# Optimization experiments

Measured on AMD Instinct MI355X. Metric: run time of the kernel, lower is better.

The kernel has to match this reference:

```python
import jax, jax.numpy as jnp
import numpy as np

D_MODEL, D_K, D_V = 1024, 128, 128


def setup_inputs() -> dict:
    key = jax.random.key(0)
    kx, kq, kk, kv = jax.random.split(key, 4)
    B, T = 8, 2048
    x = jax.random.normal(kx, (B, T, D_MODEL), dtype=jnp.float32)
    # nn.Linear(d_model, d_out, bias=False): weight [d_out, d_model], y = x @ W.T
    s = 1.0 / np.sqrt(D_MODEL)
    Wq = jax.random.uniform(kq, (D_K, D_MODEL), jnp.float32, -s, s)
    Wk = jax.random.uniform(kk, (D_K, D_MODEL), jnp.float32, -s, s)
    Wv = jax.random.uniform(kv, (D_V, D_MODEL), jnp.float32, -s, s)
    return {"x": x, "Wq": Wq, "Wk": Wk, "Wv": Wv}


def reference(x, Wq, Wk, Wv):
    B, T, C = x.shape
    Q = jnp.einsum('btc,kc->btk', x, Wq)  # [B,T,d_k]
    K = jnp.einsum('btc,kc->btk', x, Wk)  # [B,T,d_k]
    V = jnp.einsum('btc,vc->btv', x, Wv)  # [B,T,d_v]
    scores = jnp.einsum('bqk,btk->bqt', Q, K) / jnp.sqrt(jnp.float32(D_K))  # [B,T,T]
    causal = jnp.tril(jnp.ones((T, T), dtype=bool))
    scores = jnp.where(causal, scores, -jnp.inf)
    probs = jax.nn.softmax(scores, axis=2)
    return jnp.einsum('bqt,btv->bqv', probs, V)
```

## Files before the change

### kernel.cpp

```cpp
#include <hip/hip_runtime.h>
#include <hip/hip_bf16.h>

#define BATCH 8
#define TDIM  2048
#define CDIM  1024
#define DDIM  128

typedef float  f32x4  __attribute__((ext_vector_type(4)));
typedef __bf16 bf16x8 __attribute__((ext_vector_type(8)));
typedef unsigned short u16;
typedef unsigned int   u32;
typedef u16 u16x4 __attribute__((ext_vector_type(4)));
typedef u16 u16x8 __attribute__((ext_vector_type(8)));
typedef u32 u32x4 __attribute__((ext_vector_type(4)));

static __device__ __forceinline__ u16 f2bf(float f) {
    union { float f; unsigned int u; } cv;
    cv.f = f;
    unsigned int lsb = (cv.u >> 16) & 1u;
    cv.u += 0x7fffu + lsb;
    return (u16)(cv.u >> 16);
}

static __device__ __forceinline__ float bf2f(u16 v) {
    union { u32 u; float f; } cv;
    cv.u = (u32)v << 16;
    return cv.f;
}

static __device__ __forceinline__ u32 packbf(float a, float b) {
    return (u32)f2bf(a) | ((u32)f2bf(b) << 16);
}

static __device__ __forceinline__ void gload16(const u16* g, u16* l) {
    __builtin_amdgcn_global_load_lds(
        (const __attribute__((address_space(1))) void*)g,
        (__attribute__((address_space(3))) void*)l, 16, 0, 0);
}

__global__ __launch_bounds__(256) void convert_w(
    const float* __restrict__ Wq, const float* __restrict__ Wk,
    const float* __restrict__ Wv, u16* __restrict__ wb)
{
    const int which = blockIdx.x >> 4;
    const int kb    = blockIdx.x & 15;
    const float* W = (which == 0) ? Wq : (which == 1) ? Wk : Wv;
    u16* dst = wb + ((size_t)(which * 16 + kb)) * 8192;
    const int t = threadIdx.x;
    for (int i = 0; i < 4; ++i) {
        int j   = i * 256 + t;
        int row = j & 127;
        int cb  = (j >> 7) & 3;
        int kk2 = j >> 9;
        const float* s = &W[(size_t)row * CDIM + kb * 64 + kk2 * 32 + cb * 8];
        f32x4 a = *reinterpret_cast<const f32x4*>(s);
        f32x4 b = *reinterpret_cast<const f32x4*>(s + 4);
        u16x8 o;
        o[0] = f2bf(a[0]); o[1] = f2bf(a[1]); o[2] = f2bf(a[2]); o[3] = f2bf(a[3]);
        o[4] = f2bf(b[0]); o[5] = f2bf(b[1]); o[6] = f2bf(b[2]); o[7] = f2bf(b[3]);
        *reinterpret_cast<u16x8*>(dst + (size_t)j * 8) = o;
    }
}

__global__ __launch_bounds__(256) void qkv_gemm(
    const float* __restrict__ x, const u16* __restrict__ wb,
    u16* __restrict__ Qw, u16* __restrict__ Ktl, u16* __restrict__ Vtl)
{
    __shared__ alignas(16) u16 As[4096];
    __shared__ alignas(16) u16 Bs[8192];

    const int bid   = blockIdx.x;
    const int which = bid >> 8;
    const int mt    = bid & 255;
    const int rbase = mt * 64;
    const u16* Bb = wb + (size_t)which * 131072;

    const int tid  = threadIdx.x;
    const int wid  = tid >> 6;
    const int lane = tid & 63;
    const int g    = lane >> 4;
    const int lr   = lane & 15;
    const int wc   = wid * 32;

    const int arow = tid >> 2;
    const int aseg = tid & 3;
    const int abase = (aseg >> 1) * 2048 + (aseg & 1) * 1024 + arow * 8;

    f32x4 acc[4][2] = {};

    for (int kb = 0; kb < 16; ++kb) {
        const float* ax = &x[(size_t)(rbase + arow) * CDIM + kb * 64 + aseg * 16];
        f32x4 v0 = *reinterpret_cast<const f32x4*>(ax);
        f32x4 v1 = *reinterpret_cast<const f32x4*>(ax + 4);
        f32x4 v2 = *reinterpret_cast<const f32x4*>(ax + 8);
        f32x4 v3 = *reinterpret_cast<const f32x4*>(ax + 12);
        u16x8 p0, p1;
        p0[0]=f2bf(v0[0]); p0[1]=f2bf(v0[1]); p0[2]=f2bf(v0[2]); p0[3]=f2bf(v0[3]);
        p0[4]=f2bf(v1[0]); p0[5]=f2bf(v1[1]); p0[6]=f2bf(v1[2]); p0[7]=f2bf(v1[3]);
        p1[0]=f2bf(v2[0]); p1[1]=f2bf(v2[1]); p1[2]=f2bf(v2[2]); p1[3]=f2bf(v2[3]);
        p1[4]=f2bf(v3[0]); p1[5]=f2bf(v3[1]); p1[6]=f2bf(v3[2]); p1[7]=f2bf(v3[3]);
        *reinterpret_cast<u16x8*>(&As[abase])       = p0;
        *reinterpret_cast<u16x8*>(&As[abase + 512]) = p1;
        const u16* Bt = Bb + (size_t)kb * 8192;
        for (int i = 0; i < 4; ++i)
            gload16(Bt + (size_t)(i * 256 + tid) * 8, &Bs[(i * 256 + wid * 64) * 8]);
        __syncthreads();

        bf16x8 af[2][4], bf[2][2];
        for (int kk2 = 0; kk2 < 2; ++kk2) {
            for (int mi = 0; mi < 4; ++mi)
                af[kk2][mi] = __builtin_bit_cast(bf16x8, *reinterpret_cast<const u16x8*>(
                    &As[kk2 * 2048 + g * 512 + (mi * 16 + lr) * 8]));
            for (int ni = 0; ni < 2; ++ni)
                bf[kk2][ni] = __builtin_bit_cast(bf16x8, *reinterpret_cast<const u16x8*>(
                    &Bs[kk2 * 4096 + g * 1024 + (wc + ni * 16 + lr) * 8]));
        }
        for (int kk2 = 0; kk2 < 2; ++kk2)
            for (int mi = 0; mi < 4; ++mi)
                for (int ni = 0; ni < 2; ++ni)
                    acc[mi][ni] = __builtin_amdgcn_mfma_f32_16x16x32_bf16(
                        af[kk2][mi], bf[kk2][ni], acc[mi][ni], 0, 0, 0);
        __syncthreads();
    }

    const int b  = mt >> 5;
    const int kt = mt & 31;
    if (which == 0) {
        const float sc = 0.08838834764831845f;
        for (int mi = 0; mi < 4; ++mi)
            for (int ni = 0; ni < 2; ++ni) {
                int row = mi * 16 + g * 4;
                int col = wc + ni * 16 + lr;
                for (int r = 0; r < 4; ++r)
                    Bs[(row + r) * 128 + col] = f2bf(acc[mi][ni][r] * sc);
            }
        __syncthreads();
        u16* dst = Qw + (size_t)rbase * DDIM;
        for (int i = 0; i < 4; ++i)
            *reinterpret_cast<u16x8*>(&dst[(size_t)(i * 256 + tid) * 8]) =
                *reinterpret_cast<const u16x8*>(&Bs[(i * 256 + tid) * 8]);
    } else if (which == 1) {
        for (int mi = 0; mi < 4; ++mi)
            for (int ni = 0; ni < 2; ++ni) {
                int row = mi * 16 + g * 4;
                int col = wc + ni * 16 + lr;
                int ebase = (col >> 5) * 2048 + ((col >> 3) & 3) * 512 + (col & 7);
                for (int r = 0; r < 4; ++r)
                    Bs[ebase + (row + r) * 8] = f2bf(acc[mi][ni][r]);
            }
        __syncthreads();
        u16* dst = Ktl + ((size_t)(b * 32 + kt)) * 8192;
        for (int i = 0; i < 4; ++i)
            *reinterpret_cast<u16x8*>(&dst[(size_t)(i * 256 + tid) * 8]) =
                *reinterpret_cast<const u16x8*>(&Bs[(i * 256 + tid) * 8]);
    } else {
        for (int mi = 0; mi < 4; ++mi)
            for (int ni = 0; ni < 2; ++ni) {
                int row = mi * 16 + g * 4;
                int col = wc + ni * 16 + lr;
                for (int r = 0; r < 4; ++r) {
                    int t_loc = row + r;
                    Bs[(t_loc >> 5) * 4096 + ((t_loc >> 3) & 3) * 1024 +
                       col * 8 + (t_loc & 7)] = f2bf(acc[mi][ni][r]);
                }
            }
        __syncthreads();
        u16* dst = Vtl + ((size_t)(b * 32 + kt)) * 8192;
        for (int i = 0; i < 4; ++i)
            *reinterpret_cast<u16x8*>(&dst[(size_t)(i * 256 + tid) * 8]) =
                *reinterpret_cast<const u16x8*>(&Bs[(i * 256 + tid) * 8]);
    }
}

__global__ __launch_bounds__(256) void attn(
    const u16* __restrict__ Qw, const u16* __restrict__ Ktl,
    const u16* __restrict__ Vtl, float* __restrict__ out,
    u16* __restrict__ po, float* __restrict__ pm, float* __restrict__ pl)
{
    __shared__ alignas(16) u16 Ks[8192];
    __shared__ alignas(16) u16 Vs[8192];
    constexpr int LDPW = 36;
    __shared__ u32 Plw[4][16 * LDPW];

    const int s = blockIdx.x;
    const int b = blockIdx.y;
    int gg = 0;
    while (s >= 2 * (gg + 1) * (gg + 2)) ++gg;
    const int r_     = s - 2 * gg * (gg + 1);
    const int qt     = 4 * gg + r_ / (gg + 1);
    const int split  = r_ % (gg + 1);
    const int kt0 = split * 4;
    const int kt1 = min(kt0 + 4, qt + 1);

    const int tid  = threadIdx.x;
    const int wid  = tid >> 6;
    const int lane = tid & 63;
    const int g    = lane >> 4;
    const int lr   = lane & 15;
    const int qrow0 = qt * 64 + wid * 16;
    const int q = qrow0 + lr;

    const u16* Qp = Qw + ((size_t)(b * TDIM + qrow0)) * DDIM;
    bf16x8 qf[4];
    for (int kk = 0; kk < 4; ++kk)
        qf[kk] = __builtin_bit_cast(bf16x8, *reinterpret_cast<const u16x8*>(
            &Qp[lr * DDIM + kk * 32 + g * 8]));

    f32x4 o[8] = {};
    float mrow = -1e30f;
    float lsum = 0.f;
    u32* Pw = &Plw[wid][0];

    for (int kt = kt0; kt < kt1; ++kt) {
        const u16* Kt = Ktl + ((size_t)(b * 32 + kt)) * 8192;
        const u16* Vt = Vtl + ((size_t)(b * 32 + kt)) * 8192;
        for (int i = 0; i < 4; ++i)
            gload16(Kt + (size_t)(i * 256 + tid) * 8, &Ks[(i * 256 + wid * 64) * 8]);
        for (int i = 0; i < 4; ++i)
            gload16(Vt + (size_t)(i * 256 + tid) * 8, &Vs[(i * 256 + wid * 64) * 8]);
        __syncthreads();

        f32x4 sf[4] = {};
        for (int js = 0; js < 4; ++js)
            for (int kk = 0; kk < 4; ++kk) {
                bf16x8 kf = __builtin_bit_cast(bf16x8, *reinterpret_cast<const u16x8*>(
                    &Ks[kk * 2048 + g * 512 + (js * 16 + lr) * 8]));
                sf[js] = __builtin_amdgcn_mfma_f32_16x16x32_bf16(
                    kf, qf[kk], sf[js], 0, 0, 0);
            }

        float pv[4][4];
        float tmax = -1e30f;
        const bool maskt = (kt == qt);
        const int kvb = kt * 64 + g * 4;
        for (int js = 0; js < 4; ++js)
            for (int r = 0; r < 4; ++r) {
                float v = sf[js][r];
                if (maskt && (kvb + js * 16 + r) > q) v = -1e30f;
                pv[js][r] = v;
                tmax = fmaxf(tmax, v);
            }
        tmax = fmaxf(tmax, __shfl_xor(tmax, 16));
        tmax = fmaxf(tmax, __shfl_xor(tmax, 32));
        float nm = fmaxf(mrow, tmax);
        float al = __expf(mrow - nm);
        mrow = nm;
        float rs = 0.f;
        for (int js = 0; js < 4; ++js)
            for (int r = 0; r < 4; ++r) {
                float p = __expf(pv[js][r] - nm);
                pv[js][r] = p;
                rs += p;
            }
        rs += __shfl_xor(rs, 16);
        rs += __shfl_xor(rs, 32);
        lsum = lsum * al + rs;

        for (int js = 0; js < 4; ++js) {
            Pw[lr * LDPW + js * 8 + g * 2 + 0] = packbf(pv[js][0], pv[js][1]);
            Pw[lr * LDPW + js * 8 + g * 2 + 1] = packbf(pv[js][2], pv[js][3]);
        }

        float alo[4];
        for (int r = 0; r < 4; ++r)
            alo[r] = __shfl(al, g * 20 + r);
        for (int dt = 0; dt < 8; ++dt)
            for (int r = 0; r < 4; ++r)
                o[dt][r] *= alo[r];

        for (int c = 0; c < 2; ++c) {
            u32x4 prd = *reinterpret_cast<const u32x4*>(&Pw[lr * LDPW + c * 16 + g * 4]);
            bf16x8 pf = __builtin_bit_cast(bf16x8, prd);
            for (int dt = 0; dt < 8; ++dt) {
                bf16x8 vf = __builtin_bit_cast(bf16x8, *reinterpret_cast<const u16x8*>(
                    &Vs[c * 4096 + g * 1024 + (dt * 16 + lr) * 8]));
                o[dt] = __builtin_amdgcn_mfma_f32_16x16x32_bf16(
                    pf, vf, o[dt], 0, 0, 0);
            }
        }
        __syncthreads();
    }

    float linv = 1.0f / lsum;
    float linvo[4];
    for (int r = 0; r < 4; ++r)
        linvo[r] = __shfl(linv, g * 20 + r);

    if (gg == 0) {
        float* orow = out + ((size_t)(b * TDIM + qrow0)) * DDIM;
        for (int dt = 0; dt < 8; ++dt)
            for (int r = 0; r < 4; ++r)
                orow[(size_t)(g * 4 + r) * DDIM + dt * 16 + lr] = o[dt][r] * linvo[r];
    } else {
        const int slot = (b * 32 + qt) * 8 + split;
        u16* pob = po + (size_t)slot * 8192 + (size_t)(wid * 16) * 128;
        for (int dt = 0; dt < 8; ++dt)
            for (int r = 0; r < 4; ++r)
                pob[(size_t)(g * 4 + r) * 128 + dt * 16 + lr] = f2bf(o[dt][r] * linvo[r]);
        if (g == 0) {
            pm[slot * 64 + wid * 16 + lr] = mrow;
            pl[slot * 64 + wid * 16 + lr] = lsum;
        }
    }
}

__global__ __launch_bounds__(256) void combine(
    const u16* __restrict__ po, const float* __restrict__ pm,
    const float* __restrict__ pl, float* __restrict__ out)
{
    const int qt = 4 + blockIdx.x;
    const int b  = blockIdx.y;
    const int nsplit = (qt >> 2) + 1;
    const int tid = threadIdx.x;
    const int row = tid >> 2;
    const int cs  = tid & 3;
    const int slot0 = (b * 32 + qt) * 8;

    float mv[8], wv[8];
    float M = -1e30f;
    #pragma unroll 8
    for (int i = 0; i < 8; ++i)
        if (i < nsplit) { mv[i] = pm[(slot0 + i) * 64 + row]; M = fmaxf(M, mv[i]); }
    float L = 0.f;
    #pragma unroll 8
    for (int i = 0; i < 8; ++i)
        if (i < nsplit) { wv[i] = pl[(slot0 + i) * 64 + row] * __expf(mv[i] - M); L += wv[i]; }
    float invL = 1.0f / L;

    float acc[32] = {};
    #pragma unroll 8
    for (int i = 0; i < 8; ++i)
        if (i < nsplit) {
            float w = wv[i] * invL;
            const u16* pr = &po[(size_t)(slot0 + i) * 8192 + (size_t)row * 128 + cs * 32];
            for (int j2 = 0; j2 < 4; ++j2) {
                u16x8 v = *reinterpret_cast<const u16x8*>(&pr[j2 * 8]);
                for (int e = 0; e < 8; ++e)
                    acc[j2 * 8 + e] += w * bf2f(v[e]);
            }
        }
    float* orow = &out[((size_t)(b * TDIM) + qt * 64 + row) * DDIM + cs * 32];
    for (int j4 = 0; j4 < 8; ++j4) {
        f32x4 v;
        v[0] = acc[j4*4+0]; v[1] = acc[j4*4+1]; v[2] = acc[j4*4+2]; v[3] = acc[j4*4+3];
        *reinterpret_cast<f32x4*>(&orow[j4 * 4]) = v;
    }
}

extern "C" void kernel_launch(void* const* d_in, const int* in_sizes, int n_in,
                              void* d_out, int out_size, void* d_ws, size_t ws_size,
                              hipStream_t stream) {
    const float* x  = (const float*)d_in[0];
    const float* Wq = (const float*)d_in[1];
    const float* Wk = (const float*)d_in[2];
    const float* Wv = (const float*)d_in[3];
    float* out = (float*)d_out;

    char* base = (char*)d_ws;
    u16*   wb  = (u16*)base;
    u16*   Qw  = (u16*)(base + 0x100000);
    u16*   Ktl = (u16*)(base + 0x500000);
    u16*   Vtl = (u16*)(base + 0x900000);
    u16*   po  = (u16*)(base + 0xD00000);
    float* pm  = (float*)(base + 0x2D00000);
    float* pl  = (float*)(base + 0x2D80000);

    convert_w<<<dim3(48), dim3(256), 0, stream>>>(Wq, Wk, Wv, wb);
    qkv_gemm<<<dim3(768), dim3(256), 0, stream>>>(x, wb, Qw, Ktl, Vtl);
    attn<<<dim3(144, BATCH), dim3(256), 0, stream>>>(Qw, Ktl, Vtl, out, po, pm, pl);
    combine<<<dim3(28, BATCH), dim3(256), 0, stream>>>(po, pm, pl, out);
}
```

Baseline: 159.9 us.

## Double-buffer LDS tiles in QKV GEMM and attention, add lazy softmax rescale

The QKV GEMM and the attention kernel now keep two LDS buffers each. The next K-tile or KV-tile is fetched through global_load_lds, and the next x slice is converted, while MFMAs run on the current buffer, with explicit waitcnt and barriers in place of syncthreads. The attention softmax also skips the running-max update and the rescale of the O accumulator unless some row's tile max exceeds the stored max by more than 8. This aims to hide global load latency and trim per-tile exp and multiply work, at the cost of doubled LDS (which may reduce occupancy) and reliance on hand-placed vmcnt counts for correctness.

```diff
diff --git a/kernel.cpp b/kernel.cpp
--- a/kernel.cpp
+++ b/kernel.cpp
@@ -37,6 +37,9 @@
         (const __attribute__((address_space(1))) void*)g,
         (__attribute__((address_space(3))) void*)l, 16, 0, 0);
 }
+
+#define SCHED_FENCE() __builtin_amdgcn_sched_barrier(0)
+#define BARRIER()     __builtin_amdgcn_s_barrier()
 
 __global__ __launch_bounds__(256) void convert_w(
     const float* __restrict__ Wq, const float* __restrict__ Wk,
@@ -66,8 +69,8 @@
     const float* __restrict__ x, const u16* __restrict__ wb,
     u16* __restrict__ Qw, u16* __restrict__ Ktl, u16* __restrict__ Vtl)
 {
-    __shared__ alignas(16) u16 As[4096];
-    __shared__ alignas(16) u16 Bs[8192];
+    __shared__ alignas(16) u16 As[2][4096];
+    __shared__ alignas(16) u16 Bs[2][8192];
 
     const int bid   = blockIdx.x;
     const int which = bid >> 8;
@@ -85,44 +88,68 @@
     const int arow = tid >> 2;
     const int aseg = tid & 3;
     const int abase = (aseg >> 1) * 2048 + (aseg & 1) * 1024 + arow * 8;
+    const float* xrow = &x[(size_t)(rbase + arow) * CDIM + aseg * 16];
+
+    f32x4 ar[4], an[4];
+    #define LOADA(dst, kb_) { \
+        const float* ax_ = xrow + (kb_) * 64; \
+        dst[0] = *reinterpret_cast<const f32x4*>(ax_); \
+        dst[1] = *reinterpret_cast<const f32x4*>(ax_ + 4); \
+        dst[2] = *reinterpret_cast<const f32x4*>(ax_ + 8); \
+        dst[3] = *reinterpret_cast<const f32x4*>(ax_ + 12); }
+    #define CONVA(src, buf_) { \
+        u16x8 p0_, p1_; \
+        p0_[0]=f2bf(src[0][0]); p0_[1]=f2bf(src[0][1]); p0_[2]=f2bf(src[0][2]); p0_[3]=f2bf(src[0][3]); \
+        p0_[4]=f2bf(src[1][0]); p0_[5]=f2bf(src[1][1]); p0_[6]=f2bf(src[1][2]); p0_[7]=f2bf(src[1][3]); \
+        p1_[0]=f2bf(src[2][0]); p1_[1]=f2bf(src[2][1]); p1_[2]=f2bf(src[2][2]); p1_[3]=f2bf(src[2][3]); \
+        p1_[4]=f2bf(src[3][0]); p1_[5]=f2bf(src[3][1]); p1_[6]=f2bf(src[3][2]); p1_[7]=f2bf(src[3][3]); \
+        *reinterpret_cast<u16x8*>(&As[buf_][abase])       = p0_; \
+        *reinterpret_cast<u16x8*>(&As[buf_][abase + 512]) = p1_; }
+    #define LOADB(buf_, kb_) { \
+        const u16* Bt_ = Bb + (size_t)(kb_) * 8192; \
+        for (int i_ = 0; i_ < 4; ++i_) \
+            gload16(Bt_ + (size_t)(i_ * 256 + tid) * 8, &Bs[buf_][(i_ * 256 + wid * 64) * 8]); }
 
     f32x4 acc[4][2] = {};
 
+    LOADA(ar, 0);
+    LOADB(0, 0);
+    LOADA(an, 1);
+    CONVA(ar, 0);
+    asm volatile("s_waitcnt vmcnt(4) lgkmcnt(0)" ::: "memory");
+    SCHED_FENCE(); BARRIER(); SCHED_FENCE();
+
     for (int kb = 0; kb < 16; ++kb) {
-        const float* ax = &x[(size_t)(rbase + arow) * CDIM + kb * 64 + aseg * 16];
-        f32x4 v0 = *reinterpret_cast<const f32x4*>(ax);
-        f32x4 v1 = *reinterpret_cast<const f32x4*>(ax + 4);
-        f32x4 v2 = *reinterpret_cast<const f32x4*>(ax + 8);
-        f32x4 v3 = *reinterpret_cast<const f32x4*>(ax + 12);
-        u16x8 p0, p1;
-        p0[0]=f2bf(v0[0]); p0[1]=f2bf(v0[1]); p0[2]=f2bf(v0[2]); p0[3]=f2bf(v0[3]);
-        p0[4]=f2bf(v1[0]); p0[5]=f2bf(v1[1]); p0[6]=f2bf(v1[2]); p0[7]=f2bf(v1[3]);
-        p1[0]=f2bf(v2[0]); p1[1]=f2bf(v2[1]); p1[2]=f2bf(v2[2]); p1[3]=f2bf(v2[3]);
-        p1[4]=f2bf(v3[0]); p1[5]=f2bf(v3[1]); p1[6]=f2bf(v3[2]); p1[7]=f2bf(v3[3]);
-        *reinterpret_cast<u16x8*>(&As[abase])       = p0;
-        *reinterpret_cast<u16x8*>(&As[abase + 512]) = p1;
-        const u16* Bt = Bb + (size_t)kb * 8192;
-        for (int i = 0; i < 4; ++i)
-            gload16(Bt + (size_t)(i * 256 + tid) * 8, &Bs[(i * 256 + wid * 64) * 8]);
-        __syncthreads();
-
-        bf16x8 af[2][4], bf[2][2];
+        const int cur = kb & 1, nxt = cur ^ 1;
+        if (kb < 15) {
+            LOADB(nxt, kb + 1);
+            CONVA(an, nxt);
+            if (kb < 14) LOADA(an, kb + 2);
+        }
+        bf16x8 af[2][4], bfr[2][2];
         for (int kk2 = 0; kk2 < 2; ++kk2) {
             for (int mi = 0; mi < 4; ++mi)
                 af[kk2][mi] = __builtin_bit_cast(bf16x8, *reinterpret_cast<const u16x8*>(
-                    &As[kk2 * 2048 + g * 512 + (mi * 16 + lr) * 8]));
+                    &As[cur][kk2 * 2048 + g * 512 + (mi * 16 + lr) * 8]));
             for (int ni = 0; ni < 2; ++ni)
-                bf[kk2][ni] = __builtin_bit_cast(bf16x8, *reinterpret_cast<const u16x8*>(
-                    &Bs[kk2 * 4096 + g * 1024 + (wc + ni * 16 + lr) * 8]));
+                bfr[kk2][ni] = __builtin_bit_cast(bf16x8, *reinterpret_cast<const u16x8*>(
+                    &Bs[cur][kk2 * 4096 + g * 1024 + (wc + ni * 16 + lr) * 8]));
         }
         for (int kk2 = 0; kk2 < 2; ++kk2)
             for (int mi = 0; mi < 4; ++mi)
                 for (int ni = 0; ni < 2; ++ni)
                     acc[mi][ni] = __builtin_amdgcn_mfma_f32_16x16x32_bf16(
-                        af[kk2][mi], bf[kk2][ni], acc[mi][ni], 0, 0, 0);
-        __syncthreads();
-    }
-
+                        af[kk2][mi], bfr[kk2][ni], acc[mi][ni], 0, 0, 0);
+        if (kb < 14) {
+            asm volatile("s_waitcnt vmcnt(4) lgkmcnt(0)" ::: "memory");
+            SCHED_FENCE(); BARRIER(); SCHED_FENCE();
+        } else if (kb == 14) {
+            asm volatile("s_waitcnt vmcnt(0) lgkmcnt(0)" ::: "memory");
+            SCHED_FENCE(); BARRIER(); SCHED_FENCE();
+        }
+    }
+
+    u16* bnc = &Bs[0][0];
     const int b  = mt >> 5;
     const int kt = mt & 31;
     if (which == 0) {
@@ -132,13 +159,13 @@
                 int row = mi * 16 + g * 4;
                 int col = wc + ni * 16 + lr;
                 for (int r = 0; r < 4; ++r)
-                    Bs[(row + r) * 128 + col] = f2bf(acc[mi][ni][r] * sc);
+                    bnc[(row + r) * 128 + col] = f2bf(acc[mi][ni][r] * sc);
             }
         __syncthreads();
         u16* dst = Qw + (size_t)rbase * DDIM;
         for (int i = 0; i < 4; ++i)
             *reinterpret_cast<u16x8*>(&dst[(size_t)(i * 256 + tid) * 8]) =
-                *reinterpret_cast<const u16x8*>(&Bs[(i * 256 + tid) * 8]);
+                *reinterpret_cast<const u16x8*>(&bnc[(i * 256 + tid) * 8]);
     } else if (which == 1) {
         for (int mi = 0; mi < 4; ++mi)
             for (int ni = 0; ni < 2; ++ni) {
@@ -146,13 +173,13 @@
                 int col = wc + ni * 16 + lr;
                 int ebase = (col >> 5) * 2048 + ((col >> 3) & 3) * 512 + (col & 7);
                 for (int r = 0; r < 4; ++r)
-                    Bs[ebase + (row + r) * 8] = f2bf(acc[mi][ni][r]);
+                    bnc[ebase + (row + r) * 8] = f2bf(acc[mi][ni][r]);
             }
         __syncthreads();
         u16* dst = Ktl + ((size_t)(b * 32 + kt)) * 8192;
         for (int i = 0; i < 4; ++i)
             *reinterpret_cast<u16x8*>(&dst[(size_t)(i * 256 + tid) * 8]) =
-                *reinterpret_cast<const u16x8*>(&Bs[(i * 256 + tid) * 8]);
+                *reinterpret_cast<const u16x8*>(&bnc[(i * 256 + tid) * 8]);
     } else {
         for (int mi = 0; mi < 4; ++mi)
             for (int ni = 0; ni < 2; ++ni) {
@@ -160,15 +187,15 @@
                 int col = wc + ni * 16 + lr;
                 for (int r = 0; r < 4; ++r) {
                     int t_loc = row + r;
-                    Bs[(t_loc >> 5) * 4096 + ((t_loc >> 3) & 3) * 1024 +
-                       col * 8 + (t_loc & 7)] = f2bf(acc[mi][ni][r]);
+                    bnc[(t_loc >> 5) * 4096 + ((t_loc >> 3) & 3) * 1024 +
+                        col * 8 + (t_loc & 7)] = f2bf(acc[mi][ni][r]);
                 }
             }
         __syncthreads();
         u16* dst = Vtl + ((size_t)(b * 32 + kt)) * 8192;
         for (int i = 0; i < 4; ++i)
             *reinterpret_cast<u16x8*>(&dst[(size_t)(i * 256 + tid) * 8]) =
-                *reinterpret_cast<const u16x8*>(&Bs[(i * 256 + tid) * 8]);
+                *reinterpret_cast<const u16x8*>(&bnc[(i * 256 + tid) * 8]);
     }
 }
 
@@ -177,8 +204,8 @@
     const u16* __restrict__ Vtl, float* __restrict__ out,
     u16* __restrict__ po, float* __restrict__ pm, float* __restrict__ pl)
 {
-    __shared__ alignas(16) u16 Ks[8192];
-    __shared__ alignas(16) u16 Vs[8192];
+    __shared__ alignas(16) u16 Ks[2][8192];
+    __shared__ alignas(16) u16 Vs[2][8192];
     constexpr int LDPW = 36;
     __shared__ u32 Plw[4][16 * LDPW];
 
@@ -200,31 +227,40 @@
     const int qrow0 = qt * 64 + wid * 16;
     const int q = qrow0 + lr;
 
+    #define STAGEKV(buf_, kt_) { \
+        const u16* Kt_ = Ktl + ((size_t)(b * 32 + (kt_))) * 8192; \
+        const u16* Vt_ = Vtl + ((size_t)(b * 32 + (kt_))) * 8192; \
+        for (int i_ = 0; i_ < 4; ++i_) \
+            gload16(Kt_ + (size_t)(i_ * 256 + tid) * 8, &Ks[buf_][(i_ * 256 + wid * 64) * 8]); \
+        for (int i_ = 0; i_ < 4; ++i_) \
+            gload16(Vt_ + (size_t)(i_ * 256 + tid) * 8, &Vs[buf_][(i_ * 256 + wid * 64) * 8]); }
+
+    STAGEKV(0, kt0);
+
     const u16* Qp = Qw + ((size_t)(b * TDIM + qrow0)) * DDIM;
     bf16x8 qf[4];
     for (int kk = 0; kk < 4; ++kk)
         qf[kk] = __builtin_bit_cast(bf16x8, *reinterpret_cast<const u16x8*>(
             &Qp[lr * DDIM + kk * 32 + g * 8]));
 
+    asm volatile("s_waitcnt vmcnt(0)" ::: "memory");
+    SCHED_FENCE(); BARRIER(); SCHED_FENCE();
+
     f32x4 o[8] = {};
     float mrow = -1e30f;
     float lsum = 0.f;
     u32* Pw = &Plw[wid][0];
+    int cur = 0;
 
     for (int kt = kt0; kt < kt1; ++kt) {
-        const u16* Kt = Ktl + ((size_t)(b * 32 + kt)) * 8192;
-        const u16* Vt = Vtl + ((size_t)(b * 32 + kt)) * 8192;
-        for (int i = 0; i < 4; ++i)
-            gload16(Kt + (size_t)(i * 256 + tid) * 8, &Ks[(i * 256 + wid * 64) * 8]);
-        for (int i = 0; i < 4; ++i)
-            gload16(Vt + (size_t)(i * 256 + tid) * 8, &Vs[(i * 256 + wid * 64) * 8]);
-        __syncthreads();
+        const bool hasnext = (kt + 1 < kt1);
+        if (hasnext) STAGEKV(cur ^ 1, kt + 1);
 
         f32x4 sf[4] = {};
         for (int js = 0; js < 4; ++js)
             for (int kk = 0; kk < 4; ++kk) {
                 bf16x8 kf = __builtin_bit_cast(bf16x8, *reinterpret_cast<const u16x8*>(
-                    &Ks[kk * 2048 + g * 512 + (js * 16 + lr) * 8]));
+                    &Ks[cur][kk * 2048 + g * 512 + (js * 16 + lr) * 8]));
                 sf[js] = __builtin_amdgcn_mfma_f32_16x16x32_bf16(
                     kf, qf[kk], sf[js], 0, 0, 0);
             }
@@ -242,13 +278,17 @@
             }
         tmax = fmaxf(tmax, __shfl_xor(tmax, 16));
         tmax = fmaxf(tmax, __shfl_xor(tmax, 32));
-        float nm = fmaxf(mrow, tmax);
-        float al = __expf(mrow - nm);
-        mrow = nm;
+        const bool rescale = __any(tmax > mrow + 8.0f);
+        float al = 1.0f;
+        if (rescale) {
+            float nm = fmaxf(mrow, tmax);
+            al = __expf(mrow - nm);
+            mrow = nm;
+        }
         float rs = 0.f;
         for (int js = 0; js < 4; ++js)
             for (int r = 0; r < 4; ++r) {
-                float p = __expf(pv[js][r] - nm);
+                float p = __expf(pv[js][r] - mrow);
                 pv[js][r] = p;
                 rs += p;
             }
@@ -261,24 +301,31 @@
             Pw[lr * LDPW + js * 8 + g * 2 + 1] = packbf(pv[js][2], pv[js][3]);
         }
 
-        float alo[4];
-        for (int r = 0; r < 4; ++r)
-            alo[r] = __shfl(al, g * 20 + r);
-        for (int dt = 0; dt < 8; ++dt)
+        if (rescale) {
+            float alo[4];
             for (int r = 0; r < 4; ++r)
-                o[dt][r] *= alo[r];
+                alo[r] = __shfl(al, g * 20 + r);
+            for (int dt = 0; dt < 8; ++dt)
+                for (int r = 0; r < 4; ++r)
+                    o[dt][r] *= alo[r];
+        }
 
         for (int c = 0; c < 2; ++c) {
             u32x4 prd = *reinterpret_cast<const u32x4*>(&Pw[lr * LDPW + c * 16 + g * 4]);
             bf16x8 pf = __builtin_bit_cast(bf16x8, prd);
             for (int dt = 0; dt < 8; ++dt) {
                 bf16x8 vf = __builtin_bit_cast(bf16x8, *reinterpret_cast<const u16x8*>(
-                    &Vs[c * 4096 + g * 1024 + (dt * 16 + lr) * 8]));
+                    &Vs[cur][c * 4096 + g * 1024 + (dt * 16 + lr) * 8]));
                 o[dt] = __builtin_amdgcn_mfma_f32_16x16x32_bf16(
                     pf, vf, o[dt], 0, 0, 0);
             }
         }
-        __syncthreads();
+
+        if (hasnext) {
+            asm volatile("s_waitcnt vmcnt(0) lgkmcnt(0)" ::: "memory");
+            SCHED_FENCE(); BARRIER(); SCHED_FENCE();
+            cur ^= 1;
+        }
     }
 
     float linv = 1.0f / lsum;
```

Measured after the change: 169.0 us. 5.7% more time.
